# Optimization experiments

Hardware: AMD Instinct MI355X
Metric: run time of the kernel (lower is better)

Reference implementation:

```python
import jax, jax.numpy as jnp
import numpy as np

LAYERS = 3       # opt.layer
B = 4096         # batch of sessions
MAX_LEN = 200    # padded session length
N_ITEMS = 100000 # item vocab (index 0 is PAD after zero-row concat)
E = 112          # emb_size (SessConv default)
EPS = 1e-12      # F.normalize eps


def setup_inputs() -> dict:
    key = jax.random.key(0)
    k0, k1, k2, k3, k4 = jax.random.split(key, 5)
    item_embedding = jax.random.normal(k0, (N_ITEMS, E), dtype=jnp.float32) * 0.1
    # Session-session adjacency A and diagonal inverse-degree D (so D @ A is row-normalized)
    A = jax.random.uniform(k1, (B, B), dtype=jnp.float32)
    D = jnp.diag(1.0 / A.sum(axis=1))
    # Padded session item indices; 0 == PAD row (zeros prepended to the table)
    session_item = jax.random.randint(k2, (B, MAX_LEN), 0, N_ITEMS + 1, dtype=jnp.int64)
    session_len = jax.random.randint(k3, (B, 1), 1, MAX_LEN + 1).astype(jnp.float32)
    # layers x Linear(E, E, bias=False) weights, torch layout [out, in]
    Ws = jax.random.normal(k4, (LAYERS, E, E), dtype=jnp.float32) * (1.0 / np.sqrt(E))
    return {"item_embedding": item_embedding, "D": D, "A": A,
            "session_len": session_len, "Ws": Ws, "session_item": session_item}


def reference(item_embedding, D, A, session_len, Ws, session_item):
    # Prepend zero row so index 0 gathers zeros (padding)
    emb = jnp.concatenate([jnp.zeros((1, E), item_embedding.dtype), item_embedding], axis=0)
    # Fused ragged gather + mean-pool (replaces per-session index_select + cpu/numpy roundtrip)
    seq_h = emb[session_item]                       # [B, MAX_LEN, E]
    session_emb = seq_h.sum(axis=1) / session_len   # [B, E]
    DA = D @ A                                      # [B, B]
    acc = session_emb                               # layer-0 term of the final average
    for i in range(LAYERS):
        session_emb = session_emb @ Ws[i].T         # Linear(E,E,bias=False)
        session_emb = DA @ session_emb              # session graph propagation
        nrm = jnp.linalg.norm(session_emb, axis=-1, keepdims=True)
        acc = acc + session_emb / jnp.maximum(nrm, EPS)  # appended term is L2-normalized
        # NOTE: next layer consumes the UN-normalized session_emb (as in the torch code)
    return acc / (LAYERS + 1)
```

## Files before the change

kernel.cpp:

```cpp
#include <hip/hip_runtime.h>
#include <hip/hip_bf16.h>

#define BSZ 4096
#define MAXLEN 200
#define EDIM 112
#define NW 8

typedef __attribute__((ext_vector_type(8))) short bf16x8;
typedef __attribute__((ext_vector_type(4))) float f32x4;

static __device__ __forceinline__ short f2bf(float f) {
    unsigned u = __float_as_uint(f);
    unsigned r = (u + 0x7fffu + ((u >> 16) & 1u)) >> 16;
    return (short)r;
}
static __device__ __forceinline__ float bf2f(short s) {
    return __uint_as_float(((unsigned)(unsigned short)s) << 16);
}
static __device__ __forceinline__ bf16x8 cvt8(float4 a, float4 b) {
    bf16x8 r;
    r[0] = f2bf(a.x); r[1] = f2bf(a.y); r[2] = f2bf(a.z); r[3] = f2bf(a.w);
    r[4] = f2bf(b.x); r[5] = f2bf(b.y); r[6] = f2bf(b.z); r[7] = f2bf(b.w);
    return r;
}
static __device__ __forceinline__ unsigned pack2(float a, float b) {
    return ((unsigned)f2bf(a) & 0xffffu) | ((unsigned)f2bf(b) << 16);
}

__global__ __launch_bounds__(256) void f32_to_bf16(const float* __restrict__ src,
                                                   unsigned short* __restrict__ dst,
                                                   int ngroups, int zgroups) {
    int g = blockIdx.x * 256 + threadIdx.x;
    if (g >= ngroups) return;
    bf16x8 o;
    if (g < zgroups) {
        #pragma unroll
        for (int i = 0; i < 8; ++i) o[i] = 0;
    } else {
        const float* p = src + (size_t)(g - zgroups) * 8;
        float4 a = *(const float4*)p;
        float4 b = *(const float4*)(p + 4);
        o = cvt8(a, b);
    }
    *(bf16x8*)(dst + (size_t)g * 8) = o;
}

__global__ __launch_bounds__(256) void gather_pool_bf(const unsigned short* __restrict__ Ebf,
                                                      const int* __restrict__ items,
                                                      const float* __restrict__ slen,
                                                      float* __restrict__ S,
                                                      float* __restrict__ acc) {
    __shared__ float part[16][14][8];
    int wave = threadIdx.x >> 6;
    int lane = threadIdx.x & 63;
    int b = blockIdx.x;
    int rg = lane / 14;
    int c  = lane % 14;
    const int* it = items + (size_t)b * MAXLEN + wave * 50;
    float a[8];
    #pragma unroll
    for (int e = 0; e < 8; ++e) a[e] = 0.f;
    if (lane < 56) {
        #pragma unroll
        for (int t = 0; t < 13; ++t) {
            int j = t * 4 + rg;
            int idx = 0;
            if (j < 50) idx = it[j];
            bf16x8 v = *(const bf16x8*)(Ebf + (size_t)idx * EDIM + c * 8);
            #pragma unroll
            for (int e = 0; e < 8; ++e) a[e] += bf2f(v[e]);
        }
        #pragma unroll
        for (int e = 0; e < 8; ++e) part[wave * 4 + rg][c][e] = a[e];
    }
    __syncthreads();
    int tid = threadIdx.x;
    if (tid < EDIM) {
        int cc = tid >> 3, ee = tid & 7;
        float s = 0.f;
        #pragma unroll
        for (int g = 0; g < 16; ++g) s += part[g][cc][ee];
        s /= slen[b];
        S[(size_t)b * EDIM + tid]   = s;
        acc[(size_t)b * EDIM + tid] = s;
    }
}

static __device__ __forceinline__ bf16x8 ldcvt(const float* p, bool valid) {
    if (valid) {
        float4 a = *(const float4*)(p);
        float4 b = *(const float4*)(p + 4);
        return cvt8(a, b);
    }
    bf16x8 z;
    #pragma unroll
    for (int i = 0; i < 8; ++i) z[i] = 0;
    return z;
}

__global__ __launch_bounds__(64, 4) void fused_mid0(const float* __restrict__ Sin,
                                                    const float* __restrict__ W,
                                                    unsigned short* __restrict__ Bsw) {
    __shared__ unsigned short Ylds[16][136];
    int lane = threadIdx.x;
    int gw = blockIdx.x;
    int j0 = gw * 16;
    int nrow = lane & 15;
    int quad = lane >> 4;
    int ses = j0 + nrow;

    float4 v[7];
    const float4* p = (const float4*)(Sin + (size_t)ses * EDIM + quad * 28);
    #pragma unroll
    for (int i = 0; i < 7; ++i) v[i] = p[i];

    #pragma unroll
    for (int i = 0; i < 7; ++i) {
        uint2 pk;
        pk.x = pack2(v[i].x, v[i].y);
        pk.y = pack2(v[i].z, v[i].w);
        *(uint2*)&Ylds[nrow][quad * 28 + i * 4] = pk;
    }
    *(uint2*)&Ylds[nrow][112 + quad * 4] = make_uint2(0u, 0u);
    __syncthreads();

    bf16x8 aF[4];
    #pragma unroll
    for (int k32 = 0; k32 < 4; ++k32)
        aF[k32] = *(bf16x8*)&Ylds[nrow][k32 * 32 + quad * 8];

    f32x4 acc[7];
    #pragma unroll
    for (int t = 0; t < 7; ++t) acc[t] = (f32x4){0.f, 0.f, 0.f, 0.f};
    #pragma unroll
    for (int t = 0; t < 7; ++t) {
        const float* wr = W + (size_t)(16 * t + nrow) * EDIM;
        #pragma unroll
        for (int k32 = 0; k32 < 4; ++k32) {
            bf16x8 bF = ldcvt(wr + k32 * 32 + quad * 8, (k32 < 3) || (quad < 2));
            acc[t] = __builtin_amdgcn_mfma_f32_16x16x32_bf16(aF[k32], bF, acc[t], 0, 0, 0);
        }
    }

    int k32f = j0 >> 5;
    int qp = ((j0 >> 4) & 1) * 2 + (quad >> 1);
    int e0 = (quad & 1) * 4;
    #pragma unroll
    for (int t = 0; t < 7; ++t) {
        uint2 pk;
        pk.x = pack2(acc[t][0], acc[t][1]);
        pk.y = pack2(acc[t][2], acc[t][3]);
        *(uint2*)(Bsw + ((size_t)(k32f * 7 + t) * 64 + qp * 16 + nrow) * 8 + e0) = pk;
    }
}

template <int AMODE, int LAST>
__global__ __launch_bounds__(512, 2) void bg_fused(const float* __restrict__ Af,
                                                   unsigned short* __restrict__ Asw,
                                                   const unsigned short* __restrict__ Bsw,
                                                   const float* __restrict__ Dm,
                                                   float* __restrict__ accb,
                                                   const float* __restrict__ W,
                                                   unsigned short* __restrict__ BswOut,
                                                   float* __restrict__ out) {
    __shared__ float part[NW][16][116];
    __shared__ unsigned short Ylds[16][136];
    int tid = threadIdx.x;
    int w = tid >> 6;
    int lane = tid & 63;
    int nrow = lane & 15;
    int quad = lane >> 4;
    int mtile = blockIdx.x;

    f32x4 acc[7];
    #pragma unroll
    for (int t = 0; t < 7; ++t) acc[t] = (f32x4){0.f, 0.f, 0.f, 0.f};

    auto LOADA = [&](int k32) -> bf16x8 {
        size_t afrag = ((size_t)(mtile * 128 + k32) * 64 + lane) * 8;
        if (AMODE == 0) {
            const float* p = Af + (size_t)(mtile * 16 + nrow) * 4096 + k32 * 32 + quad * 8;
            float4 a0 = *(const float4*)p;
            float4 a1 = *(const float4*)(p + 4);
            bf16x8 r = cvt8(a0, a1);
            *(bf16x8*)(Asw + afrag) = r;
            return r;
        } else {
            return *(const bf16x8*)(Asw + afrag);
        }
    };

    int k32 = w * 16;
    bf16x8 aF = LOADA(k32);
    bf16x8 bF[7];
    {
        const unsigned short* bb = Bsw + ((size_t)k32 * 7 * 64 + lane) * 8;
        #pragma unroll
        for (int t = 0; t < 7; ++t) bF[t] = *(const bf16x8*)(bb + (size_t)t * 512);
    }
    #pragma unroll 1
    for (int ks = 0; ks < 15; ++ks) {
        bf16x8 aN = LOADA(k32 + 1);
        bf16x8 bN[7];
        const unsigned short* bb = Bsw + ((size_t)(k32 + 1) * 7 * 64 + lane) * 8;
        #pragma unroll
        for (int t = 0; t < 7; ++t) bN[t] = *(const bf16x8*)(bb + (size_t)t * 512);
        #pragma unroll
        for (int t = 0; t < 7; ++t)
            acc[t] = __builtin_amdgcn_mfma_f32_16x16x32_bf16(aF, bF[t], acc[t], 0, 0, 0);
        aF = aN;
        #pragma unroll
        for (int t = 0; t < 7; ++t) bF[t] = bN[t];
        ++k32;
    }
    #pragma unroll
    for (int t = 0; t < 7; ++t)
        acc[t] = __builtin_amdgcn_mfma_f32_16x16x32_bf16(aF, bF[t], acc[t], 0, 0, 0);

    #pragma unroll
    for (int t = 0; t < 7; ++t)
        #pragma unroll
        for (int r = 0; r < 4; ++r)
            part[w][quad * 4 + r][16 * t + nrow] = acc[t][r];
    __syncthreads();

    int half = lane >> 5;
    int cg = lane & 31;
    int row = 2 * w + half;
    int grow = mtile * 16 + row;
    int col = cg * 4;
    float4 v = make_float4(0.f, 0.f, 0.f, 0.f);
    if (cg < 28) {
        #pragma unroll
        for (int p = 0; p < NW; ++p) {
            float4 t = *(const float4*)&part[p][row][col];
            v.x += t.x; v.y += t.y; v.z += t.z; v.w += t.w;
        }
    }
    float d = Dm[(size_t)grow * (BSZ + 1)];
    v.x *= d; v.y *= d; v.z *= d; v.w *= d;
    float ss = v.x * v.x + v.y * v.y + v.z * v.z + v.w * v.w;
    ss += __shfl_xor(ss, 1, 64);
    ss += __shfl_xor(ss, 2, 64);
    ss += __shfl_xor(ss, 4, 64);
    ss += __shfl_xor(ss, 8, 64);
    ss += __shfl_xor(ss, 16, 64);
    float rinv = 1.f / fmaxf(sqrtf(ss), 1e-12f);
    if (cg < 28) {
        if (LAST) {
            float4 a = *(const float4*)(accb + (size_t)grow * EDIM + col);
            float4 o;
            o.x = (a.x + v.x * rinv) * 0.25f;
            o.y = (a.y + v.y * rinv) * 0.25f;
            o.z = (a.z + v.z * rinv) * 0.25f;
            o.w = (a.w + v.w * rinv) * 0.25f;
            *(float4*)(out + (size_t)grow * EDIM + col) = o;
        } else {
            float4* pa = (float4*)(accb + (size_t)grow * EDIM + col);
            float4 a = *pa;
            a.x += v.x * rinv; a.y += v.y * rinv;
            a.z += v.z * rinv; a.w += v.w * rinv;
            *pa = a;
        }
    }

    if (!LAST) {
        uint2 pk;
        pk.x = pack2(v.x, v.y);
        pk.y = pack2(v.z, v.w);
        *(uint2*)&Ylds[row][col] = pk;
        __syncthreads();

        if (w < 7) {
            int t = w;
            bf16x8 aF2[4];
            #pragma unroll
            for (int k = 0; k < 4; ++k)
                aF2[k] = *(bf16x8*)&Ylds[nrow][k * 32 + quad * 8];
            f32x4 c = (f32x4){0.f, 0.f, 0.f, 0.f};
            const float* wr = W + (size_t)(16 * t + nrow) * EDIM;
            #pragma unroll
            for (int k = 0; k < 4; ++k) {
                bf16x8 bW = ldcvt(wr + k * 32 + quad * 8, (k < 3) || (quad < 2));
                c = __builtin_amdgcn_mfma_f32_16x16x32_bf16(aF2[k], bW, c, 0, 0, 0);
            }
            int j0 = mtile * 16;
            int k32f = j0 >> 5;
            int qp = ((j0 >> 4) & 1) * 2 + (quad >> 1);
            int e0 = (quad & 1) * 4;
            uint2 ck;
            ck.x = pack2(c[0], c[1]);
            ck.y = pack2(c[2], c[3]);
            *(uint2*)(BswOut + ((size_t)(k32f * 7 + t) * 64 + qp * 16 + nrow) * 8 + e0) = ck;
        }
    }
}

extern "C" void kernel_launch(void* const* d_in, const int* in_sizes, int n_in,
                              void* d_out, int out_size, void* d_ws, size_t ws_size,
                              hipStream_t stream) {
    (void)in_sizes; (void)n_in; (void)out_size; (void)ws_size;
    const float* emb   = (const float*)d_in[0];
    const float* Dm    = (const float*)d_in[1];
    const float* A     = (const float*)d_in[2];
    const float* slen  = (const float*)d_in[3];
    const float* Ws    = (const float*)d_in[4];
    const int*   items = (const int*)d_in[5];
    float* out = (float*)d_out;

    char* w = (char*)d_ws;
    float* Sa   = (float*)w;
    float* accb = Sa + BSZ * EDIM;
    unsigned short* Bsw0 = (unsigned short*)(accb + BSZ * EDIM);
    unsigned short* Bsw1 = Bsw0 + (size_t)128 * 7 * 64 * 8;
    unsigned short* Ebf  = Bsw1 + (size_t)128 * 7 * 64 * 8;
    unsigned short* Asw  = Ebf + (size_t)100001 * EDIM;

    f32_to_bf16<<<5470, 256, 0, stream>>>(emb, Ebf, 1400014, 14);
    gather_pool_bf<<<BSZ, 256, 0, stream>>>(Ebf, items, slen, Sa, accb);
    fused_mid0<<<256, 64, 0, stream>>>(Sa, Ws, Bsw0);
    bg_fused<0, 0><<<256, 512, 0, stream>>>(A, Asw, Bsw0, Dm, accb,
                                            Ws + (size_t)EDIM * EDIM, Bsw1, nullptr);
    bg_fused<1, 0><<<256, 512, 0, stream>>>(nullptr, Asw, Bsw1, Dm, accb,
                                            Ws + (size_t)2 * EDIM * EDIM, Bsw0, nullptr);
    bg_fused<1, 1><<<256, 512, 0, stream>>>(nullptr, Asw, Bsw0, Dm, accb,
                                            nullptr, nullptr, out);
}
```

Baseline: 253.7 us.

## Pipeline DA-propagation GEMM through LDS with async global loads, move A conversion to prep

Moves the fp32-to-bf16 swizzle of A out of the first layer kernel into a combined prep kernel that also converts the embedding table. The layer kernel changes from per-wave split-K with an LDS partial-sum reduction to one output tile per wave. A and B fragments are staged through a 4-deep LDS ring filled by global_load_lds and synchronised with vmcnt waits and barriers. This removes the cross-wave reduction and register double-buffering, at the cost of one wave acting only as a loader and a barrier on every k-step.

```diff
diff --git a/kernel.cpp b/kernel.cpp
--- a/kernel.cpp
+++ b/kernel.cpp
@@ -4,7 +4,10 @@
 #define BSZ 4096
 #define MAXLEN 200
 #define EDIM 112
-#define NW 8
+
+#define TBL_GROUPS 1400014
+#define TBL_ZGROUPS 14
+#define AFRAG_JOBS (256 * 128 * 64)
 
 typedef __attribute__((ext_vector_type(8))) short bf16x8;
 typedef __attribute__((ext_vector_type(4))) float f32x4;
@@ -27,22 +30,41 @@
     return ((unsigned)f2bf(a) & 0xffffu) | ((unsigned)f2bf(b) << 16);
 }
 
-__global__ __launch_bounds__(256) void f32_to_bf16(const float* __restrict__ src,
-                                                   unsigned short* __restrict__ dst,
-                                                   int ngroups, int zgroups) {
+static __device__ __forceinline__ void glds16(const unsigned short* g, unsigned short* l) {
+    __builtin_amdgcn_global_load_lds(
+        (__attribute__((address_space(1))) void*)(void*)g,
+        (__attribute__((address_space(3))) void*)l, 16, 0, 0);
+}
+
+__global__ __launch_bounds__(256) void prep(const float* __restrict__ emb,
+                                            unsigned short* __restrict__ Ebf,
+                                            const float* __restrict__ Af,
+                                            unsigned short* __restrict__ Asw) {
     int g = blockIdx.x * 256 + threadIdx.x;
-    if (g >= ngroups) return;
-    bf16x8 o;
-    if (g < zgroups) {
-        #pragma unroll
-        for (int i = 0; i < 8; ++i) o[i] = 0;
+    if (g < TBL_GROUPS) {
+        bf16x8 o;
+        if (g < TBL_ZGROUPS) {
+            #pragma unroll
+            for (int i = 0; i < 8; ++i) o[i] = 0;
+        } else {
+            const float* p = emb + (size_t)(g - TBL_ZGROUPS) * 8;
+            float4 a = *(const float4*)p;
+            float4 b = *(const float4*)(p + 4);
+            o = cvt8(a, b);
+        }
+        *(bf16x8*)(Ebf + (size_t)g * 8) = o;
     } else {
-        const float* p = src + (size_t)(g - zgroups) * 8;
-        float4 a = *(const float4*)p;
-        float4 b = *(const float4*)(p + 4);
-        o = cvt8(a, b);
-    }
-    *(bf16x8*)(dst + (size_t)g * 8) = o;
+        int g2 = g - TBL_GROUPS;
+        if (g2 >= AFRAG_JOBS) return;
+        int lane = g2 & 63;
+        int k32 = (g2 >> 6) & 127;
+        int M16 = g2 >> 13;
+        int nrow = lane & 15, quad = lane >> 4;
+        const float* p = Af + (size_t)(M16 * 16 + nrow) * BSZ + k32 * 32 + quad * 8;
+        float4 a0 = *(const float4*)p;
+        float4 a1 = *(const float4*)(p + 4);
+        *(bf16x8*)(Asw + (((size_t)M16 * 128 + k32) * 64 + lane) * 8) = cvt8(a0, a1);
+    }
 }
 
 __global__ __launch_bounds__(256) void gather_pool_bf(const unsigned short* __restrict__ Ebf,
@@ -154,17 +176,21 @@
     }
 }
 
-template <int AMODE, int LAST>
-__global__ __launch_bounds__(512, 2) void bg_fused(const float* __restrict__ Af,
-                                                   unsigned short* __restrict__ Asw,
+template <int LAST>
+__global__ __launch_bounds__(512, 1) void bg_layer(const unsigned short* __restrict__ Asw,
                                                    const unsigned short* __restrict__ Bsw,
                                                    const float* __restrict__ Dm,
                                                    float* __restrict__ accb,
                                                    const float* __restrict__ W,
                                                    unsigned short* __restrict__ BswOut,
                                                    float* __restrict__ out) {
-    __shared__ float part[NW][16][116];
+    __shared__ unsigned short Abuf[4][2][512];
+    __shared__ unsigned short Bbuf[4][2][7][512];
     __shared__ unsigned short Ylds[16][136];
+    __shared__ float sqp[7][16];
+    __shared__ float rinvl[16];
+    __shared__ float dl[16];
+
     int tid = threadIdx.x;
     int w = tid >> 6;
     int lane = tid & 63;
@@ -172,105 +198,103 @@
     int quad = lane >> 4;
     int mtile = blockIdx.x;
 
-    f32x4 acc[7];
-    #pragma unroll
-    for (int t = 0; t < 7; ++t) acc[t] = (f32x4){0.f, 0.f, 0.f, 0.f};
-
-    auto LOADA = [&](int k32) -> bf16x8 {
-        size_t afrag = ((size_t)(mtile * 128 + k32) * 64 + lane) * 8;
-        if (AMODE == 0) {
-            const float* p = Af + (size_t)(mtile * 16 + nrow) * 4096 + k32 * 32 + quad * 8;
-            float4 a0 = *(const float4*)p;
-            float4 a1 = *(const float4*)(p + 4);
-            bf16x8 r = cvt8(a0, a1);
-            *(bf16x8*)(Asw + afrag) = r;
-            return r;
+    if (tid < 16) dl[tid] = Dm[(size_t)(mtile * 16 + tid) * (BSZ + 1)];
+    __syncthreads();
+
+    f32x4 acc = (f32x4){0.f, 0.f, 0.f, 0.f};
+
+    auto STAGE = [&](int s, int buf) {
+        int k0 = 2 * s;
+        if (w == 7) {
+            #pragma unroll
+            for (int j = 0; j < 2; ++j)
+                glds16(Asw + (((size_t)mtile * 128 + k0 + j) * 64 + lane) * 8,
+                       &Abuf[buf][j][0]);
         } else {
-            return *(const bf16x8*)(Asw + afrag);
+            #pragma unroll
+            for (int j = 0; j < 2; ++j)
+                glds16(Bsw + (((size_t)(k0 + j) * 7 + w) * 64 + lane) * 8,
+                       &Bbuf[buf][j][w][0]);
         }
     };
-
-    int k32 = w * 16;
-    bf16x8 aF = LOADA(k32);
-    bf16x8 bF[7];
-    {
-        const unsigned short* bb = Bsw + ((size_t)k32 * 7 * 64 + lane) * 8;
-        #pragma unroll
-        for (int t = 0; t < 7; ++t) bF[t] = *(const bf16x8*)(bb + (size_t)t * 512);
-    }
+    auto COMP = [&](int cur) {
+        if (w < 7) {
+            #pragma unroll
+            for (int j = 0; j < 2; ++j) {
+                bf16x8 aF = *(bf16x8*)&Abuf[cur][j][lane * 8];
+                bf16x8 bF = *(bf16x8*)&Bbuf[cur][j][w][lane * 8];
+                acc = __builtin_amdgcn_mfma_f32_16x16x32_bf16(aF, bF, acc, 0, 0, 0);
+            }
+        }
+    };
+
+    STAGE(0, 0); STAGE(1, 1); STAGE(2, 2);
     #pragma unroll 1
-    for (int ks = 0; ks < 15; ++ks) {
-        bf16x8 aN = LOADA(k32 + 1);
-        bf16x8 bN[7];
-        const unsigned short* bb = Bsw + ((size_t)(k32 + 1) * 7 * 64 + lane) * 8;
-        #pragma unroll
-        for (int t = 0; t < 7; ++t) bN[t] = *(const bf16x8*)(bb + (size_t)t * 512);
-        #pragma unroll
-        for (int t = 0; t < 7; ++t)
-            acc[t] = __builtin_amdgcn_mfma_f32_16x16x32_bf16(aF, bF[t], acc[t], 0, 0, 0);
-        aF = aN;
-        #pragma unroll
-        for (int t = 0; t < 7; ++t) bF[t] = bN[t];
-        ++k32;
-    }
-    #pragma unroll
-    for (int t = 0; t < 7; ++t)
-        acc[t] = __builtin_amdgcn_mfma_f32_16x16x32_bf16(aF, bF[t], acc[t], 0, 0, 0);
-
-    #pragma unroll
-    for (int t = 0; t < 7; ++t)
-        #pragma unroll
-        for (int r = 0; r < 4; ++r)
-            part[w][quad * 4 + r][16 * t + nrow] = acc[t][r];
-    __syncthreads();
-
-    int half = lane >> 5;
-    int cg = lane & 31;
-    int row = 2 * w + half;
-    int grow = mtile * 16 + row;
-    int col = cg * 4;
-    float4 v = make_float4(0.f, 0.f, 0.f, 0.f);
-    if (cg < 28) {
-        #pragma unroll
-        for (int p = 0; p < NW; ++p) {
-            float4 t = *(const float4*)&part[p][row][col];
-            v.x += t.x; v.y += t.y; v.z += t.z; v.w += t.w;
-        }
-    }
-    float d = Dm[(size_t)grow * (BSZ + 1)];
-    v.x *= d; v.y *= d; v.z *= d; v.w *= d;
-    float ss = v.x * v.x + v.y * v.y + v.z * v.z + v.w * v.w;
-    ss += __shfl_xor(ss, 1, 64);
-    ss += __shfl_xor(ss, 2, 64);
-    ss += __shfl_xor(ss, 4, 64);
-    ss += __shfl_xor(ss, 8, 64);
-    ss += __shfl_xor(ss, 16, 64);
-    float rinv = 1.f / fmaxf(sqrtf(ss), 1e-12f);
-    if (cg < 28) {
-        if (LAST) {
-            float4 a = *(const float4*)(accb + (size_t)grow * EDIM + col);
-            float4 o;
-            o.x = (a.x + v.x * rinv) * 0.25f;
-            o.y = (a.y + v.y * rinv) * 0.25f;
-            o.z = (a.z + v.z * rinv) * 0.25f;
-            o.w = (a.w + v.w * rinv) * 0.25f;
-            *(float4*)(out + (size_t)grow * EDIM + col) = o;
-        } else {
-            float4* pa = (float4*)(accb + (size_t)grow * EDIM + col);
-            float4 a = *pa;
-            a.x += v.x * rinv; a.y += v.y * rinv;
-            a.z += v.z * rinv; a.w += v.w * rinv;
-            *pa = a;
-        }
-    }
-
+    for (int s = 0; s < 61; ++s) {
+        asm volatile("s_waitcnt vmcnt(4)" ::: "memory");
+        __builtin_amdgcn_s_barrier();
+        STAGE(s + 3, (s + 3) & 3);
+        COMP(s & 3);
+    }
+    asm volatile("s_waitcnt vmcnt(4)" ::: "memory");
+    __builtin_amdgcn_s_barrier();
+    COMP(1);
+    asm volatile("s_waitcnt vmcnt(2)" ::: "memory");
+    __builtin_amdgcn_s_barrier();
+    COMP(2);
+    asm volatile("s_waitcnt vmcnt(0)" ::: "memory");
+    __builtin_amdgcn_s_barrier();
+    COMP(3);
+
+    float vv[4];
+    if (w < 7) {
+        float sqv[4];
+        #pragma unroll
+        for (int r = 0; r < 4; ++r) {
+            vv[r] = acc[r] * dl[quad * 4 + r];
+            sqv[r] = vv[r] * vv[r];
+        }
+        #pragma unroll
+        for (int off = 1; off < 16; off <<= 1) {
+            #pragma unroll
+            for (int r = 0; r < 4; ++r) sqv[r] += __shfl_xor(sqv[r], off, 64);
+        }
+        if ((lane & 15) == 0) {
+            #pragma unroll
+            for (int r = 0; r < 4; ++r) sqp[w][quad * 4 + r] = sqv[r];
+        }
+    }
+    __syncthreads();
+    if (tid < 16) {
+        float t = 0.f;
+        #pragma unroll
+        for (int u = 0; u < 7; ++u) t += sqp[u][tid];
+        rinvl[tid] = 1.f / fmaxf(sqrtf(t), 1e-12f);
+    }
+    __syncthreads();
+    if (w < 7) {
+        #pragma unroll
+        for (int r = 0; r < 4; ++r) {
+            int row = quad * 4 + r;
+            int col = 16 * w + nrow;
+            float y = vv[r];
+            float nv = y * rinvl[row];
+            size_t o = (size_t)(mtile * 16 + row) * EDIM + col;
+            if (LAST) {
+                out[o] = (accb[o] + nv) * 0.25f;
+            } else {
+                accb[o] += nv;
+                Ylds[row][col] = (unsigned short)f2bf(y);
+            }
+        }
+    }
     if (!LAST) {
-        uint2 pk;
-        pk.x = pack2(v.x, v.y);
-        pk.y = pack2(v.z, v.w);
-        *(uint2*)&Ylds[row][col] = pk;
+        if (w == 7) {
+            int row = lane >> 2;
+            int c0 = 112 + (lane & 3) * 4;
+            *(uint2*)&Ylds[row][c0] = make_uint2(0u, 0u);
+        }
         __syncthreads();
-
         if (w < 7) {
             int t = w;
             bf16x8 aF2[4];
@@ -316,13 +340,13 @@
     unsigned short* Ebf  = Bsw1 + (size_t)128 * 7 * 64 * 8;
     unsigned short* Asw  = Ebf + (size_t)100001 * EDIM;
 
-    f32_to_bf16<<<5470, 256, 0, stream>>>(emb, Ebf, 1400014, 14);
+    prep<<<13661, 256, 0, stream>>>(emb, Ebf, A, Asw);
     gather_pool_bf<<<BSZ, 256, 0, stream>>>(Ebf, items, slen, Sa, accb);
     fused_mid0<<<256, 64, 0, stream>>>(Sa, Ws, Bsw0);
-    bg_fused<0, 0><<<256, 512, 0, stream>>>(A, Asw, Bsw0, Dm, accb,
-                                            Ws + (size_t)EDIM * EDIM, Bsw1, nullptr);
-    bg_fused<1, 0><<<256, 512, 0, stream>>>(nullptr, Asw, Bsw1, Dm, accb,
-                                            Ws + (size_t)2 * EDIM * EDIM, Bsw0, nullptr);
-    bg_fused<1, 1><<<256, 512, 0, stream>>>(nullptr, Asw, Bsw0, Dm, accb,
-                                            nullptr, nullptr, out);
-}
+    bg_layer<0><<<256, 512, 0, stream>>>(Asw, Bsw0, Dm, accb,
+                                         Ws + (size_t)EDIM * EDIM, Bsw1, nullptr);
+    bg_layer<0><<<256, 512, 0, stream>>>(Asw, Bsw1, Dm, accb,
+                                         Ws + (size_t)2 * EDIM * EDIM, Bsw0, nullptr);
+    bg_layer<1><<<256, 512, 0, stream>>>(Asw, Bsw0, Dm, accb,
+                                         nullptr, nullptr, out);
+}
```

After: 320.5 us. 26.3% more time.
